# Kernel tuning notes

Hardware: AMD Instinct MI355X
Metric: run time of the kernel (lower is better)

Reference implementation:

```python
import jax, jax.numpy as jnp
import numpy as np

# ---- fixed hyperparameters (match init_kwargs / internal constants) ----
N_INP, N_HID = 96, 2048
DT = 0.075
GAMMA, EPSILON = 2.7, 4.7
RHO = 0.99
INPUT_SCALING = 1.0
LIF_TAU_M = 0.5
SPIKE_GAIN = 5.0
THETA_LIF, THETA_RF = 1.0, 1.0
ALPHA, BETA = 0.0, 0.0   # fixed internally (reset scaling disabled)
TAU_REF = 0.25


def setup_inputs() -> dict:
    key = jax.random.key(0)
    k_x, k_x2h, k_h2h, k_b = jax.random.split(key, 4)
    x = jax.random.normal(k_x, (32, 1024, N_INP), dtype=jnp.float32)
    # x2h = rand(n_inp, n_hid) * input_scaling
    x2h = jax.random.uniform(k_x2h, (N_INP, N_HID), dtype=jnp.float32) * INPUT_SCALING
    # h2h = 2*(2*rand - 1), then spectral-norm scaled so spectral radius = rho
    h2h = 2.0 * (2.0 * jax.random.uniform(k_h2h, (N_HID, N_HID), dtype=jnp.float32) - 1.0)
    sr = float(np.max(np.abs(np.linalg.eigvals(np.asarray(h2h, dtype=np.float64)))))
    h2h = h2h * (RHO / sr)
    # bias = (rand*2 - 1)*0.2 + 0.05
    bias = (jax.random.uniform(k_b, (N_HID,), dtype=jnp.float32) * 2.0 - 1.0) * 0.2 + 0.05
    return {"x": x, "x2h": x2h, "h2h": h2h, "bias": bias}


def reference(x, x2h, h2h, bias):
    B, T, _ = x.shape
    dt = jnp.float32(DT)
    ref_decay = jnp.exp(jnp.float32(-DT / TAU_REF))
    zeros = jnp.zeros((B, N_HID), dtype=x.dtype)
    # carry: (hy, hz, s, lif_v, ref_period, spike_counts)
    init = (zeros, zeros, zeros, zeros, zeros, zeros)

    def step(carry, xt):
        hy, hz, s, lif_v, ref_period, cnt = carry
        input_current = xt @ x2h + s @ h2h + bias          # [B, n_hid]
        lif_v = lif_v + dt * (-lif_v / LIF_TAU_M + input_current)
        lif_s = (lif_v > THETA_LIF).astype(x.dtype)
        lif_v = lif_v - lif_s * THETA_LIF
        drive = SPIKE_GAIN * lif_s
        hz = hz + dt * (drive - GAMMA * hy - EPSILON * hz)
        hy = hy + dt * hz
        s = (hy - THETA_RF - ref_period > 0).astype(x.dtype)
        hy = hy * (1.0 - s * ALPHA)
        hz = hz * (1.0 - s * BETA)
        ref_period = ref_period * ref_decay + s
        cnt = cnt + s
        return (hy, hz, s, lif_v, ref_period, cnt), None

    xt_seq = jnp.swapaxes(x, 0, 1)                          # [T, B, n_inp]
    (_, _, _, _, _, spike_counts), _ = jax.lax.scan(step, init, xt_seq)
    return spike_counts / jnp.float32(T)
```

## Files before the change

### kernel.cpp

```cpp
#include <hip/hip_runtime.h>
#include <cmath>

#define NH 2048
#define NI 96

__global__ __launch_bounds__(256) void xin_gemm(
    const float* __restrict__ A,
    const float* __restrict__ Bm,
    float* __restrict__ C)
{
    __shared__ float At[96][68];
    __shared__ float Bt[96][68];
    const int tid = threadIdx.x;
    const int rowBase = blockIdx.y * 64;
    const int colBase = blockIdx.x * 64;

    {
        const int r = tid >> 2;
        const int sub = tid & 3;
        const float4* Arow = reinterpret_cast<const float4*>(A + (size_t)(rowBase + r) * NI);
        #pragma unroll
        for (int q = 0; q < 6; ++q) {
            const int k4 = sub + 4 * q;
            float4 v = Arow[k4];
            At[k4 * 4 + 0][r] = v.x;
            At[k4 * 4 + 1][r] = v.y;
            At[k4 * 4 + 2][r] = v.z;
            At[k4 * 4 + 3][r] = v.w;
        }
    }
    {
        const int c4 = tid & 15;
        const int k0 = tid >> 4;
        #pragma unroll
        for (int g = 0; g < 6; ++g) {
            const int kk = k0 + 16 * g;
            float4 v = *reinterpret_cast<const float4*>(Bm + (size_t)kk * NH + colBase + c4 * 4);
            *reinterpret_cast<float4*>(&Bt[kk][c4 * 4]) = v;
        }
    }
    __syncthreads();

    const int ty = tid >> 4, tx = tid & 15;
    float acc[4][4] = {};
    #pragma unroll 8
    for (int kk = 0; kk < 96; ++kk) {
        float4 a = *reinterpret_cast<const float4*>(&At[kk][ty * 4]);
        float4 b = *reinterpret_cast<const float4*>(&Bt[kk][tx * 4]);
        acc[0][0] += a.x * b.x; acc[0][1] += a.x * b.y; acc[0][2] += a.x * b.z; acc[0][3] += a.x * b.w;
        acc[1][0] += a.y * b.x; acc[1][1] += a.y * b.y; acc[1][2] += a.y * b.z; acc[1][3] += a.y * b.w;
        acc[2][0] += a.z * b.x; acc[2][1] += a.z * b.y; acc[2][2] += a.z * b.z; acc[2][3] += a.z * b.w;
        acc[3][0] += a.w * b.x; acc[3][1] += a.w * b.y; acc[3][2] += a.w * b.z; acc[3][3] += a.w * b.w;
    }
    #pragma unroll
    for (int i = 0; i < 4; ++i) {
        float4 o;
        o.x = acc[i][0]; o.y = acc[i][1]; o.z = acc[i][2]; o.w = acc[i][3];
        *reinterpret_cast<float4*>(C + (size_t)(rowBase + ty * 4 + i) * NH + colBase + tx * 4) = o;
    }
}

template <int USE_XIN>
__global__ __launch_bounds__(512) void esn_seq(
    const float* __restrict__ xin,
    const float* __restrict__ x,
    const float* __restrict__ x2h,
    const float* __restrict__ h2h,
    const float* __restrict__ bias,
    float* __restrict__ out,
    int T)
{
    const int b = blockIdx.x;
    const int tid = threadIdx.x;
    const int n0 = tid * 4;
    const int wv = tid >> 6;
    const int lane = tid & 63;

    __shared__ alignas(16) int list[NH];
    __shared__ alignas(16) int wcnt[8];
    __shared__ float xt[NI];
    __shared__ alignas(16) float xstage[2][4][NH];

    constexpr float DT = 0.075f;
    constexpr float TAU_M = 0.5f;
    constexpr float GGAMMA = 2.7f;
    constexpr float GEPS = 4.7f;
    constexpr float GAIN = 5.0f;
    const float ref_decay = expf(-0.075f / 0.25f);

    float lv[4] = {0.f, 0.f, 0.f, 0.f};
    float hy[4] = {0.f, 0.f, 0.f, 0.f};
    float hz[4] = {0.f, 0.f, 0.f, 0.f};
    float rf[4] = {0.f, 0.f, 0.f, 0.f};
    float cnt[4] = {0.f, 0.f, 0.f, 0.f};
    float bs[4];
    {
        const float4 b4 = *reinterpret_cast<const float4*>(&bias[n0]);
        bs[0] = b4.x; bs[1] = b4.y; bs[2] = b4.z; bs[3] = b4.w;
    }
    int nact = 0;

    const float* __restrict__ xrow = USE_XIN ? (xin + (size_t)b * T * NH + n0) : xin;

    float4 P0, P1, P2, P3;

    if (USE_XIN) {
        #pragma unroll
        for (int r = 0; r < 4; ++r) {
            float4 v = *reinterpret_cast<const float4*>(xrow + (size_t)r * NH);
            *reinterpret_cast<float4*>(&xstage[0][r][n0]) = v;
        }
        P0 = *reinterpret_cast<const float4*>(xrow + (size_t)4 * NH);
        P1 = *reinterpret_cast<const float4*>(xrow + (size_t)5 * NH);
        P2 = *reinterpret_cast<const float4*>(xrow + (size_t)6 * NH);
        P3 = *reinterpret_cast<const float4*>(xrow + (size_t)7 * NH);
    } else {
        if (tid < NI) xt[tid] = x[(size_t)b * T * NI + tid];
    }
    __syncthreads();

    const unsigned long long below = (1ull << lane) - 1ull;
    const unsigned long long lo32 = 0xFFFFFFFFull;
    const unsigned long long mb = (lane >= 32) ? (below & ~lo32) : below;

    const int4* __restrict__ L4 = reinterpret_cast<const int4*>(list);

#define ISSUE(St, grp) do {                                                              \
        I##St = L4[(grp)];                                                               \
        const float* pr0 = h2h + (size_t)__builtin_amdgcn_readfirstlane(I##St.x) * NH;   \
        const float* pr1 = h2h + (size_t)__builtin_amdgcn_readfirstlane(I##St.y) * NH;   \
        const float* pr2 = h2h + (size_t)__builtin_amdgcn_readfirstlane(I##St.z) * NH;   \
        const float* pr3 = h2h + (size_t)__builtin_amdgcn_readfirstlane(I##St.w) * NH;   \
        W##St##_0 = *reinterpret_cast<const float4*>(pr0 + n0);                          \
        W##St##_1 = *reinterpret_cast<const float4*>(pr1 + n0);                          \
        W##St##_2 = *reinterpret_cast<const float4*>(pr2 + n0);                          \
        W##St##_3 = *reinterpret_cast<const float4*>(pr3 + n0);                          \
    } while (0)
#define ACC(St) do {                                                                  \
        a0[0] += W##St##_0.x; a0[1] += W##St##_0.y; a0[2] += W##St##_0.z; a0[3] += W##St##_0.w; \
        a1[0] += W##St##_1.x; a1[1] += W##St##_1.y; a1[2] += W##St##_1.z; a1[3] += W##St##_1.w; \
        a2[0] += W##St##_2.x; a2[1] += W##St##_2.y; a2[2] += W##St##_2.z; a2[3] += W##St##_2.w; \
        a3[0] += W##St##_3.x; a3[1] += W##St##_3.y; a3[2] += W##St##_3.z; a3[3] += W##St##_3.w; \
    } while (0)

    for (int t = 0; t < T; ++t) {
        float4 xi;
        if (USE_XIN) xi = *reinterpret_cast<const float4*>(&xstage[(t >> 2) & 1][t & 3][n0]);

        float a0[4] = {0.f, 0.f, 0.f, 0.f};
        float a1[4] = {0.f, 0.f, 0.f, 0.f};
        float a2[4] = {0.f, 0.f, 0.f, 0.f};
        float a3[4] = {0.f, 0.f, 0.f, 0.f};

        const int n4 = nact & ~3;
        const int G = n4 >> 2;
        const int tc = nact - n4;

        int4 I0, I1, I2, I3;
        float4 W0_0, W0_1, W0_2, W0_3;
        float4 W1_0, W1_1, W1_2, W1_3;
        float4 W2_0, W2_1, W2_2, W2_3;
        float4 W3_0, W3_1, W3_2, W3_3;

        if (0 < G) ISSUE(0, 0);
        if (1 < G) ISSUE(1, 1);
        if (2 < G) ISSUE(2, 2);
        if (3 < G) ISSUE(3, 3);
        float4 tw0, tw1, tw2;
        if (tc > 0) {
            const float* p = h2h + (size_t)__builtin_amdgcn_readfirstlane(list[n4]) * NH;
            tw0 = *reinterpret_cast<const float4*>(p + n0);
        }
        if (tc > 1) {
            const float* p = h2h + (size_t)__builtin_amdgcn_readfirstlane(list[n4 + 1]) * NH;
            tw1 = *reinterpret_cast<const float4*>(p + n0);
        }
        if (tc > 2) {
            const float* p = h2h + (size_t)__builtin_amdgcn_readfirstlane(list[n4 + 2]) * NH;
            tw2 = *reinterpret_cast<const float4*>(p + n0);
        }

        int g = 0;
        for (; g + 4 <= G; g += 4) {
            const bool r0 = (g + 4 < G), r1 = (g + 5 < G), r2 = (g + 6 < G), r3 = (g + 7 < G);
            ACC(0); if (r0) ISSUE(0, g + 4);
            ACC(1); if (r1) ISSUE(1, g + 5);
            ACC(2); if (r2) ISSUE(2, g + 6);
            ACC(3); if (r3) ISSUE(3, g + 7);
        }
        if (g + 0 < G) ACC(0);
        if (g + 1 < G) ACC(1);
        if (g + 2 < G) ACC(2);
        if (tc > 0) { a0[0] += tw0.x; a0[1] += tw0.y; a0[2] += tw0.z; a0[3] += tw0.w; }
        if (tc > 1) { a0[0] += tw1.x; a0[1] += tw1.y; a0[2] += tw1.z; a0[3] += tw1.w; }
        if (tc > 2) { a0[0] += tw2.x; a0[1] += tw2.y; a0[2] += tw2.z; a0[3] += tw2.w; }

        float ic[4];
        if (USE_XIN) {
            const float xiv[4] = {xi.x, xi.y, xi.z, xi.w};
            #pragma unroll
            for (int c = 0; c < 4; ++c) {
                const float rec = (a0[c] + a1[c]) + (a2[c] + a3[c]);
                ic[c] = (xiv[c] + rec) + bs[c];
            }
        } else {
            float m[4] = {0.f, 0.f, 0.f, 0.f};
            for (int i = 0; i < NI; ++i) {
                const float xv = xt[i];
                const float4 w = *reinterpret_cast<const float4*>(&x2h[(size_t)i * NH + n0]);
                m[0] += xv * w.x; m[1] += xv * w.y; m[2] += xv * w.z; m[3] += xv * w.w;
            }
            #pragma unroll
            for (int c = 0; c < 4; ++c) {
                const float rec = (a0[c] + a1[c]) + (a2[c] + a3[c]);
                ic[c] = (m[c] + rec) + bs[c];
            }
        }

        float s[4];
        #pragma unroll
        for (int c = 0; c < 4; ++c) {
            lv[c] = lv[c] + DT * (-lv[c] / TAU_M + ic[c]);
            const float ls = lv[c] > 1.0f ? 1.0f : 0.0f;
            lv[c] -= ls;
            hz[c] = hz[c] + DT * ((GAIN * ls - GGAMMA * hy[c]) - GEPS * hz[c]);
            hy[c] = hy[c] + DT * hz[c];
            s[c] = ((hy[c] - 1.0f) - rf[c]) > 0.0f ? 1.0f : 0.0f;
            rf[c] = rf[c] * ref_decay + s[c];
            cnt[c] += s[c];
        }

        const unsigned long long ba = __ballot(s[0] > 0.0f);
        const unsigned long long bb = __ballot(s[1] > 0.0f);
        const unsigned long long bc = __ballot(s[2] > 0.0f);
        const unsigned long long bd = __ballot(s[3] > 0.0f);
        if (lane == 0)
            wcnt[wv] = (int)(__popcll(ba) + __popcll(bb) + __popcll(bc) + __popcll(bd));

        if (USE_XIN && ((t & 3) == 3)) {
            const int bufW = ((t >> 2) + 1) & 1;
            *reinterpret_cast<float4*>(&xstage[bufW][0][n0]) = P0;
            *reinterpret_cast<float4*>(&xstage[bufW][1][n0]) = P1;
            *reinterpret_cast<float4*>(&xstage[bufW][2][n0]) = P2;
            *reinterpret_cast<float4*>(&xstage[bufW][3][n0]) = P3;
            const int cNext = (t >> 2) + 2;
            if (cNext * 4 + 3 < T) {
                P0 = *reinterpret_cast<const float4*>(xrow + (size_t)(cNext * 4 + 0) * NH);
                P1 = *reinterpret_cast<const float4*>(xrow + (size_t)(cNext * 4 + 1) * NH);
                P2 = *reinterpret_cast<const float4*>(xrow + (size_t)(cNext * 4 + 2) * NH);
                P3 = *reinterpret_cast<const float4*>(xrow + (size_t)(cNext * 4 + 3) * NH);
            }
        }
        __syncthreads();

        const int4 c0 = *reinterpret_cast<const int4*>(&wcnt[0]);
        const int4 c1 = *reinterpret_cast<const int4*>(&wcnt[4]);
        int pre = 0;
        pre += (wv > 0) ? c0.x : 0;
        pre += (wv > 1) ? c0.y : 0;
        pre += (wv > 2) ? c0.z : 0;
        pre += (wv > 3) ? c0.w : 0;
        pre += (wv > 4) ? c1.x : 0;
        pre += (wv > 5) ? c1.y : 0;
        pre += (wv > 6) ? c1.z : 0;
        const int tot = ((c0.x + c0.y) + (c0.z + c0.w)) + ((c1.x + c1.y) + (c1.z + c1.w));

        const int gaLo = (int)__popcll(ba & lo32);
        const int gbLo = (int)__popcll(bb & lo32);
        const int gcLo = (int)__popcll(bc & lo32);
        const int gdLo = (int)__popcll(bd & lo32);
        const int g0 = gaLo + gcLo;
        const int g1 = gbLo + gdLo;
        const int g2 = (int)(__popcll(ba) + __popcll(bc)) - g0;
        const int base02 = (lane < 32) ? 0 : (g0 + g1);
        const int base13 = (lane < 32) ? g0 : ((g0 + g1) + g2);
        const int pa = (int)__popcll(ba & mb);
        const int pb = (int)__popcll(bb & mb);
        const int pc = (int)__popcll(bc & mb);
        const int pd = (int)__popcll(bd & mb);
        const int o02 = pre + base02 + pa + pc;
        const int o13 = pre + base13 + pb + pd;
        if (s[0] > 0.0f) list[o02] = n0;
        if (s[2] > 0.0f) list[o02 + (int)((ba >> lane) & 1ull)] = n0 + 2;
        if (s[1] > 0.0f) list[o13] = n0 + 1;
        if (s[3] > 0.0f) list[o13 + (int)((bb >> lane) & 1ull)] = n0 + 3;
        nact = tot;
        if (!USE_XIN) {
            if (t + 1 < T && tid < NI) xt[tid] = x[((size_t)b * T + (t + 1)) * NI + tid];
        }
        __syncthreads();
    }
#undef ISSUE
#undef ACC

    float4 o;
    o.x = cnt[0] / (float)T;
    o.y = cnt[1] / (float)T;
    o.z = cnt[2] / (float)T;
    o.w = cnt[3] / (float)T;
    *reinterpret_cast<float4*>(out + (size_t)b * NH + n0) = o;
}

extern "C" void kernel_launch(void* const* d_in, const int* in_sizes, int n_in,
                              void* d_out, int out_size, void* d_ws, size_t ws_size,
                              hipStream_t stream) {
    const float* x    = (const float*)d_in[0];
    const float* x2h  = (const float*)d_in[1];
    const float* h2h  = (const float*)d_in[2];
    const float* bias = (const float*)d_in[3];
    float* out = (float*)d_out;

    const int M = in_sizes[0] / NI;
    const int T = 1024;
    const int B = M / T;

    const size_t xin_bytes = (size_t)M * NH * sizeof(float);
    if (ws_size >= xin_bytes) {
        float* xin = (float*)d_ws;
        dim3 grid(NH / 64, M / 64);
        xin_gemm<<<grid, 256, 0, stream>>>(x, x2h, xin);
        esn_seq<1><<<B, 512, 0, stream>>>(xin, x, x2h, h2h, bias, out, T);
    } else {
        esn_seq<0><<<B, 512, 0, stream>>>(x , x, x2h, h2h, bias, out, T);
    }
}
```

Baseline: 1.122 ms.

## Process two batch sequences per workgroup with interleaved sparse gathers

```diff
diff --git a/kernel.cpp b/kernel.cpp
--- a/kernel.cpp
+++ b/kernel.cpp
@@ -61,7 +61,340 @@
 }
 
 template <int USE_XIN>
-__global__ __launch_bounds__(512) void esn_seq(
+__global__ __launch_bounds__(512, 2) void esn_dual(
+    const float* __restrict__ xin,
+    const float* __restrict__ x,
+    const float* __restrict__ x2h,
+    const float* __restrict__ h2h,
+    const float* __restrict__ bias,
+    float* __restrict__ out,
+    int T)
+{
+    const int tid = threadIdx.x;
+    const int n0 = tid * 4;
+    const int wv = tid >> 6;
+    const int lane = tid & 63;
+    const int b0 = blockIdx.x * 2;
+
+    __shared__ alignas(16) int list[2][NH];
+    __shared__ alignas(16) int wcnt[2][8];
+    __shared__ float xt[2][NI];
+    __shared__ alignas(16) float xstage[2][2][2][NH];
+
+    constexpr float DT = 0.075f;
+    constexpr float TAU_M = 0.5f;
+    constexpr float GGAMMA = 2.7f;
+    constexpr float GEPS = 4.7f;
+    constexpr float GAIN = 5.0f;
+    const float ref_decay = expf(-0.075f / 0.25f);
+
+    float lvA[4] = {0,0,0,0}, hyA[4] = {0,0,0,0}, hzA[4] = {0,0,0,0};
+    float rfA[4] = {0,0,0,0}, cntA[4] = {0,0,0,0};
+    float lvB[4] = {0,0,0,0}, hyB[4] = {0,0,0,0}, hzB[4] = {0,0,0,0};
+    float rfB[4] = {0,0,0,0}, cntB[4] = {0,0,0,0};
+    float bs[4];
+    {
+        const float4 b4 = *reinterpret_cast<const float4*>(&bias[n0]);
+        bs[0] = b4.x; bs[1] = b4.y; bs[2] = b4.z; bs[3] = b4.w;
+    }
+    int nactA = 0, nactB = 0;
+
+    const float* __restrict__ xrowA = USE_XIN ? (xin + (size_t)b0 * T * NH + n0) : xin;
+    const float* __restrict__ xrowB = USE_XIN ? (xin + (size_t)(b0 + 1) * T * NH + n0) : xin;
+
+    float4 PA0, PA1, PB0, PB1;
+
+    if (USE_XIN) {
+        *reinterpret_cast<float4*>(&xstage[0][0][0][n0]) = *reinterpret_cast<const float4*>(xrowA + 0 * NH);
+        *reinterpret_cast<float4*>(&xstage[0][0][1][n0]) = *reinterpret_cast<const float4*>(xrowA + 1 * NH);
+        *reinterpret_cast<float4*>(&xstage[1][0][0][n0]) = *reinterpret_cast<const float4*>(xrowB + 0 * NH);
+        *reinterpret_cast<float4*>(&xstage[1][0][1][n0]) = *reinterpret_cast<const float4*>(xrowB + 1 * NH);
+        PA0 = *reinterpret_cast<const float4*>(xrowA + 2 * NH);
+        PA1 = *reinterpret_cast<const float4*>(xrowA + 3 * NH);
+        PB0 = *reinterpret_cast<const float4*>(xrowB + 2 * NH);
+        PB1 = *reinterpret_cast<const float4*>(xrowB + 3 * NH);
+    } else {
+        if (tid < NI) {
+            xt[0][tid] = x[(size_t)b0 * T * NI + tid];
+            xt[1][tid] = x[(size_t)(b0 + 1) * T * NI + tid];
+        }
+    }
+    __syncthreads();
+
+    const unsigned long long below = (1ull << lane) - 1ull;
+    const unsigned long long lo32 = 0xFFFFFFFFull;
+    const unsigned long long mb = (lane >= 32) ? (below & ~lo32) : below;
+
+    const int4* __restrict__ L4A = reinterpret_cast<const int4*>(&list[0][0]);
+    const int4* __restrict__ L4B = reinterpret_cast<const int4*>(&list[1][0]);
+
+#define ISSUE2(St, i) do {                                                               \
+        const int bt_ = ((i) < m2) ? ((i) & 1) : extraBt;                                \
+        const int gr_ = ((i) < m2) ? ((i) >> 1) : (mG + (i) - m2);                       \
+        BT##St = bt_;                                                                    \
+        I##St = bt_ ? L4B[gr_] : L4A[gr_];                                               \
+        const float* pr0 = h2h + (size_t)__builtin_amdgcn_readfirstlane(I##St.x) * NH;   \
+        const float* pr1 = h2h + (size_t)__builtin_amdgcn_readfirstlane(I##St.y) * NH;   \
+        const float* pr2 = h2h + (size_t)__builtin_amdgcn_readfirstlane(I##St.z) * NH;   \
+        const float* pr3 = h2h + (size_t)__builtin_amdgcn_readfirstlane(I##St.w) * NH;   \
+        W##St##_0 = *reinterpret_cast<const float4*>(pr0 + n0);                          \
+        W##St##_1 = *reinterpret_cast<const float4*>(pr1 + n0);                          \
+        W##St##_2 = *reinterpret_cast<const float4*>(pr2 + n0);                          \
+        W##St##_3 = *reinterpret_cast<const float4*>(pr3 + n0);                          \
+    } while (0)
+#define ACC2(St) do {                                                                    \
+        if (BT##St == 0) {                                                               \
+            aA0[0] += W##St##_0.x; aA0[1] += W##St##_0.y; aA0[2] += W##St##_0.z; aA0[3] += W##St##_0.w; \
+            aA1[0] += W##St##_1.x; aA1[1] += W##St##_1.y; aA1[2] += W##St##_1.z; aA1[3] += W##St##_1.w; \
+            aA2[0] += W##St##_2.x; aA2[1] += W##St##_2.y; aA2[2] += W##St##_2.z; aA2[3] += W##St##_2.w; \
+            aA3[0] += W##St##_3.x; aA3[1] += W##St##_3.y; aA3[2] += W##St##_3.z; aA3[3] += W##St##_3.w; \
+        } else {                                                                         \
+            aB0[0] += W##St##_0.x; aB0[1] += W##St##_0.y; aB0[2] += W##St##_0.z; aB0[3] += W##St##_0.w; \
+            aB1[0] += W##St##_1.x; aB1[1] += W##St##_1.y; aB1[2] += W##St##_1.z; aB1[3] += W##St##_1.w; \
+            aB2[0] += W##St##_2.x; aB2[1] += W##St##_2.y; aB2[2] += W##St##_2.z; aB2[3] += W##St##_2.w; \
+            aB3[0] += W##St##_3.x; aB3[1] += W##St##_3.y; aB3[2] += W##St##_3.z; aB3[3] += W##St##_3.w; \
+        }                                                                                \
+    } while (0)
+
+    for (int t = 0; t < T; ++t) {
+        float4 xiA, xiB;
+        if (USE_XIN) {
+            xiA = *reinterpret_cast<const float4*>(&xstage[0][(t >> 1) & 1][t & 1][n0]);
+            xiB = *reinterpret_cast<const float4*>(&xstage[1][(t >> 1) & 1][t & 1][n0]);
+        }
+
+        float aA0[4] = {0,0,0,0}, aA1[4] = {0,0,0,0}, aA2[4] = {0,0,0,0}, aA3[4] = {0,0,0,0};
+        float aB0[4] = {0,0,0,0}, aB1[4] = {0,0,0,0}, aB2[4] = {0,0,0,0}, aB3[4] = {0,0,0,0};
+
+        const int n4A = nactA & ~3, GA = n4A >> 2, tcA = nactA - n4A;
+        const int n4B = nactB & ~3, GB = n4B >> 2, tcB = nactB - n4B;
+        const int mG = (GA < GB) ? GA : GB;
+        const int m2 = 2 * mG;
+        const int NT = GA + GB;
+        const int extraBt = (GA > GB) ? 0 : 1;
+
+        int4 I0, I1, I2, I3;
+        int BT0, BT1, BT2, BT3;
+        float4 W0_0, W0_1, W0_2, W0_3;
+        float4 W1_0, W1_1, W1_2, W1_3;
+        float4 W2_0, W2_1, W2_2, W2_3;
+        float4 W3_0, W3_1, W3_2, W3_3;
+
+        if (0 < NT) ISSUE2(0, 0);
+        if (1 < NT) ISSUE2(1, 1);
+        if (2 < NT) ISSUE2(2, 2);
+        if (3 < NT) ISSUE2(3, 3);
+        float4 twA0, twA1, twA2, twB0, twB1, twB2;
+        if (tcA > 0) {
+            const float* p = h2h + (size_t)__builtin_amdgcn_readfirstlane(list[0][n4A]) * NH;
+            twA0 = *reinterpret_cast<const float4*>(p + n0);
+        }
+        if (tcA > 1) {
+            const float* p = h2h + (size_t)__builtin_amdgcn_readfirstlane(list[0][n4A + 1]) * NH;
+            twA1 = *reinterpret_cast<const float4*>(p + n0);
+        }
+        if (tcA > 2) {
+            const float* p = h2h + (size_t)__builtin_amdgcn_readfirstlane(list[0][n4A + 2]) * NH;
+            twA2 = *reinterpret_cast<const float4*>(p + n0);
+        }
+        if (tcB > 0) {
+            const float* p = h2h + (size_t)__builtin_amdgcn_readfirstlane(list[1][n4B]) * NH;
+            twB0 = *reinterpret_cast<const float4*>(p + n0);
+        }
+        if (tcB > 1) {
+            const float* p = h2h + (size_t)__builtin_amdgcn_readfirstlane(list[1][n4B + 1]) * NH;
+            twB1 = *reinterpret_cast<const float4*>(p + n0);
+        }
+        if (tcB > 2) {
+            const float* p = h2h + (size_t)__builtin_amdgcn_readfirstlane(list[1][n4B + 2]) * NH;
+            twB2 = *reinterpret_cast<const float4*>(p + n0);
+        }
+
+        int tk = 0;
+        for (; tk + 4 <= NT; tk += 4) {
+            ACC2(0); if (tk + 4 < NT) ISSUE2(0, tk + 4);
+            ACC2(1); if (tk + 5 < NT) ISSUE2(1, tk + 5);
+            ACC2(2); if (tk + 6 < NT) ISSUE2(2, tk + 6);
+            ACC2(3); if (tk + 7 < NT) ISSUE2(3, tk + 7);
+        }
+        if (tk + 0 < NT) ACC2(0);
+        if (tk + 1 < NT) ACC2(1);
+        if (tk + 2 < NT) ACC2(2);
+        if (tcA > 0) { aA0[0] += twA0.x; aA0[1] += twA0.y; aA0[2] += twA0.z; aA0[3] += twA0.w; }
+        if (tcA > 1) { aA0[0] += twA1.x; aA0[1] += twA1.y; aA0[2] += twA1.z; aA0[3] += twA1.w; }
+        if (tcA > 2) { aA0[0] += twA2.x; aA0[1] += twA2.y; aA0[2] += twA2.z; aA0[3] += twA2.w; }
+        if (tcB > 0) { aB0[0] += twB0.x; aB0[1] += twB0.y; aB0[2] += twB0.z; aB0[3] += twB0.w; }
+        if (tcB > 1) { aB0[0] += twB1.x; aB0[1] += twB1.y; aB0[2] += twB1.z; aB0[3] += twB1.w; }
+        if (tcB > 2) { aB0[0] += twB2.x; aB0[1] += twB2.y; aB0[2] += twB2.z; aB0[3] += twB2.w; }
+
+        float icA[4], icB[4];
+        if (USE_XIN) {
+            const float xivA[4] = {xiA.x, xiA.y, xiA.z, xiA.w};
+            const float xivB[4] = {xiB.x, xiB.y, xiB.z, xiB.w};
+            #pragma unroll
+            for (int c = 0; c < 4; ++c) {
+                const float recA = (aA0[c] + aA1[c]) + (aA2[c] + aA3[c]);
+                icA[c] = (xivA[c] + recA) + bs[c];
+                const float recB = (aB0[c] + aB1[c]) + (aB2[c] + aB3[c]);
+                icB[c] = (xivB[c] + recB) + bs[c];
+            }
+        } else {
+            float mA[4] = {0,0,0,0}, mB[4] = {0,0,0,0};
+            for (int i = 0; i < NI; ++i) {
+                const float xvA = xt[0][i];
+                const float xvB = xt[1][i];
+                const float4 w = *reinterpret_cast<const float4*>(&x2h[(size_t)i * NH + n0]);
+                mA[0] += xvA * w.x; mA[1] += xvA * w.y; mA[2] += xvA * w.z; mA[3] += xvA * w.w;
+                mB[0] += xvB * w.x; mB[1] += xvB * w.y; mB[2] += xvB * w.z; mB[3] += xvB * w.w;
+            }
+            #pragma unroll
+            for (int c = 0; c < 4; ++c) {
+                const float recA = (aA0[c] + aA1[c]) + (aA2[c] + aA3[c]);
+                icA[c] = (mA[c] + recA) + bs[c];
+                const float recB = (aB0[c] + aB1[c]) + (aB2[c] + aB3[c]);
+                icB[c] = (mB[c] + recB) + bs[c];
+            }
+        }
+
+        float sA[4], sB[4];
+        #pragma unroll
+        for (int c = 0; c < 4; ++c) {
+            lvA[c] = lvA[c] + DT * (-lvA[c] / TAU_M + icA[c]);
+            const float lsA = lvA[c] > 1.0f ? 1.0f : 0.0f;
+            lvA[c] -= lsA;
+            hzA[c] = hzA[c] + DT * ((GAIN * lsA - GGAMMA * hyA[c]) - GEPS * hzA[c]);
+            hyA[c] = hyA[c] + DT * hzA[c];
+            sA[c] = ((hyA[c] - 1.0f) - rfA[c]) > 0.0f ? 1.0f : 0.0f;
+            rfA[c] = rfA[c] * ref_decay + sA[c];
+            cntA[c] += sA[c];
+
+            lvB[c] = lvB[c] + DT * (-lvB[c] / TAU_M + icB[c]);
+            const float lsB = lvB[c] > 1.0f ? 1.0f : 0.0f;
+            lvB[c] -= lsB;
+            hzB[c] = hzB[c] + DT * ((GAIN * lsB - GGAMMA * hyB[c]) - GEPS * hzB[c]);
+            hyB[c] = hyB[c] + DT * hzB[c];
+            sB[c] = ((hyB[c] - 1.0f) - rfB[c]) > 0.0f ? 1.0f : 0.0f;
+            rfB[c] = rfB[c] * ref_decay + sB[c];
+            cntB[c] += sB[c];
+        }
+
+        const unsigned long long baA = __ballot(sA[0] > 0.0f);
+        const unsigned long long bbA = __ballot(sA[1] > 0.0f);
+        const unsigned long long bcA = __ballot(sA[2] > 0.0f);
+        const unsigned long long bdA = __ballot(sA[3] > 0.0f);
+        const unsigned long long baB = __ballot(sB[0] > 0.0f);
+        const unsigned long long bbB = __ballot(sB[1] > 0.0f);
+        const unsigned long long bcB = __ballot(sB[2] > 0.0f);
+        const unsigned long long bdB = __ballot(sB[3] > 0.0f);
+        if (lane == 0) {
+            wcnt[0][wv] = (int)(__popcll(baA) + __popcll(bbA) + __popcll(bcA) + __popcll(bdA));
+            wcnt[1][wv] = (int)(__popcll(baB) + __popcll(bbB) + __popcll(bcB) + __popcll(bdB));
+        }
+
+        if (USE_XIN && ((t & 1) == 1)) {
+            const int bufW = ((t >> 1) + 1) & 1;
+            *reinterpret_cast<float4*>(&xstage[0][bufW][0][n0]) = PA0;
+            *reinterpret_cast<float4*>(&xstage[0][bufW][1][n0]) = PA1;
+            *reinterpret_cast<float4*>(&xstage[1][bufW][0][n0]) = PB0;
+            *reinterpret_cast<float4*>(&xstage[1][bufW][1][n0]) = PB1;
+            const int cN = (t >> 1) + 2;
+            if (cN * 2 + 1 < T) {
+                PA0 = *reinterpret_cast<const float4*>(xrowA + (size_t)(cN * 2 + 0) * NH);
+                PA1 = *reinterpret_cast<const float4*>(xrowA + (size_t)(cN * 2 + 1) * NH);
+                PB0 = *reinterpret_cast<const float4*>(xrowB + (size_t)(cN * 2 + 0) * NH);
+                PB1 = *reinterpret_cast<const float4*>(xrowB + (size_t)(cN * 2 + 1) * NH);
+            }
+        }
+        __syncthreads();
+
+        {
+            const int4 c0 = *reinterpret_cast<const int4*>(&wcnt[0][0]);
+            const int4 c1 = *reinterpret_cast<const int4*>(&wcnt[0][4]);
+            int pre = 0;
+            pre += (wv > 0) ? c0.x : 0;
+            pre += (wv > 1) ? c0.y : 0;
+            pre += (wv > 2) ? c0.z : 0;
+            pre += (wv > 3) ? c0.w : 0;
+            pre += (wv > 4) ? c1.x : 0;
+            pre += (wv > 5) ? c1.y : 0;
+            pre += (wv > 6) ? c1.z : 0;
+            nactA = ((c0.x + c0.y) + (c0.z + c0.w)) + ((c1.x + c1.y) + (c1.z + c1.w));
+
+            const int gaLo = (int)__popcll(baA & lo32);
+            const int gbLo = (int)__popcll(bbA & lo32);
+            const int gcLo = (int)__popcll(bcA & lo32);
+            const int gdLo = (int)__popcll(bdA & lo32);
+            const int g0 = gaLo + gcLo;
+            const int g1 = gbLo + gdLo;
+            const int g2 = (int)(__popcll(baA) + __popcll(bcA)) - g0;
+            const int base02 = (lane < 32) ? 0 : (g0 + g1);
+            const int base13 = (lane < 32) ? g0 : ((g0 + g1) + g2);
+            const int pa = (int)__popcll(baA & mb);
+            const int pb = (int)__popcll(bbA & mb);
+            const int pc = (int)__popcll(bcA & mb);
+            const int pd = (int)__popcll(bdA & mb);
+            const int o02 = pre + base02 + pa + pc;
+            const int o13 = pre + base13 + pb + pd;
+            if (sA[0] > 0.0f) list[0][o02] = n0;
+            if (sA[2] > 0.0f) list[0][o02 + (int)((baA >> lane) & 1ull)] = n0 + 2;
+            if (sA[1] > 0.0f) list[0][o13] = n0 + 1;
+            if (sA[3] > 0.0f) list[0][o13 + (int)((bbA >> lane) & 1ull)] = n0 + 3;
+        }
+        {
+            const int4 c0 = *reinterpret_cast<const int4*>(&wcnt[1][0]);
+            const int4 c1 = *reinterpret_cast<const int4*>(&wcnt[1][4]);
+            int pre = 0;
+            pre += (wv > 0) ? c0.x : 0;
+            pre += (wv > 1) ? c0.y : 0;
+            pre += (wv > 2) ? c0.z : 0;
+            pre += (wv > 3) ? c0.w : 0;
+            pre += (wv > 4) ? c1.x : 0;
+            pre += (wv > 5) ? c1.y : 0;
+            pre += (wv > 6) ? c1.z : 0;
+            nactB = ((c0.x + c0.y) + (c0.z + c0.w)) + ((c1.x + c1.y) + (c1.z + c1.w));
+
+            const int gaLo = (int)__popcll(baB & lo32);
+            const int gbLo = (int)__popcll(bbB & lo32);
+            const int gcLo = (int)__popcll(bcB & lo32);
+            const int gdLo = (int)__popcll(bdB & lo32);
+            const int g0 = gaLo + gcLo;
+            const int g1 = gbLo + gdLo;
+            const int g2 = (int)(__popcll(baB) + __popcll(bcB)) - g0;
+            const int base02 = (lane < 32) ? 0 : (g0 + g1);
+            const int base13 = (lane < 32) ? g0 : ((g0 + g1) + g2);
+            const int pa = (int)__popcll(baB & mb);
+            const int pb = (int)__popcll(bbB & mb);
+            const int pc = (int)__popcll(bcB & mb);
+            const int pd = (int)__popcll(bdB & mb);
+            const int o02 = pre + base02 + pa + pc;
+            const int o13 = pre + base13 + pb + pd;
+            if (sB[0] > 0.0f) list[1][o02] = n0;
+            if (sB[2] > 0.0f) list[1][o02 + (int)((baB >> lane) & 1ull)] = n0 + 2;
+            if (sB[1] > 0.0f) list[1][o13] = n0 + 1;
+            if (sB[3] > 0.0f) list[1][o13 + (int)((bbB >> lane) & 1ull)] = n0 + 3;
+        }
+        if (!USE_XIN) {
+            if (t + 1 < T && tid < NI) {
+                xt[0][tid] = x[((size_t)b0 * T + (t + 1)) * NI + tid];
+                xt[1][tid] = x[((size_t)(b0 + 1) * T + (t + 1)) * NI + tid];
+            }
+        }
+        __syncthreads();
+    }
+#undef ISSUE2
+#undef ACC2
+
+    float4 oA, oB;
+    oA.x = cntA[0] / (float)T; oA.y = cntA[1] / (float)T;
+    oA.z = cntA[2] / (float)T; oA.w = cntA[3] / (float)T;
+    oB.x = cntB[0] / (float)T; oB.y = cntB[1] / (float)T;
+    oB.z = cntB[2] / (float)T; oB.w = cntB[3] / (float)T;
+    *reinterpret_cast<float4*>(out + (size_t)b0 * NH + n0) = oA;
+    *reinterpret_cast<float4*>(out + (size_t)(b0 + 1) * NH + n0) = oB;
+}
+
+template <int USE_XIN>
+__global__ __launch_bounds__(512) void esn_seq1(
     const float* __restrict__ xin,
     const float* __restrict__ x,
     const float* __restrict__ x2h,
@@ -88,11 +421,8 @@
     constexpr float GAIN = 5.0f;
     const float ref_decay = expf(-0.075f / 0.25f);
 
-    float lv[4] = {0.f, 0.f, 0.f, 0.f};
-    float hy[4] = {0.f, 0.f, 0.f, 0.f};
-    float hz[4] = {0.f, 0.f, 0.f, 0.f};
-    float rf[4] = {0.f, 0.f, 0.f, 0.f};
-    float cnt[4] = {0.f, 0.f, 0.f, 0.f};
+    float lv[4] = {0,0,0,0}, hy[4] = {0,0,0,0}, hz[4] = {0,0,0,0};
+    float rf[4] = {0,0,0,0}, cnt[4] = {0,0,0,0};
     float bs[4];
     {
         const float4 b4 = *reinterpret_cast<const float4*>(&bias[n0]);
@@ -101,7 +431,6 @@
     int nact = 0;
 
     const float* __restrict__ xrow = USE_XIN ? (xin + (size_t)b * T * NH + n0) : xin;
-
     float4 P0, P1, P2, P3;
 
     if (USE_XIN) {
@@ -122,10 +451,9 @@
     const unsigned long long below = (1ull << lane) - 1ull;
     const unsigned long long lo32 = 0xFFFFFFFFull;
     const unsigned long long mb = (lane >= 32) ? (below & ~lo32) : below;
-
     const int4* __restrict__ L4 = reinterpret_cast<const int4*>(list);
 
-#define ISSUE(St, grp) do {                                                              \
+#define ISSUE1(St, grp) do {                                                             \
         I##St = L4[(grp)];                                                               \
         const float* pr0 = h2h + (size_t)__builtin_amdgcn_readfirstlane(I##St.x) * NH;   \
         const float* pr1 = h2h + (size_t)__builtin_amdgcn_readfirstlane(I##St.y) * NH;   \
@@ -136,7 +464,7 @@
         W##St##_2 = *reinterpret_cast<const float4*>(pr2 + n0);                          \
         W##St##_3 = *reinterpret_cast<const float4*>(pr3 + n0);                          \
     } while (0)
-#define ACC(St) do {                                                                  \
+#define ACC1(St) do {                                                                    \
         a0[0] += W##St##_0.x; a0[1] += W##St##_0.y; a0[2] += W##St##_0.z; a0[3] += W##St##_0.w; \
         a1[0] += W##St##_1.x; a1[1] += W##St##_1.y; a1[2] += W##St##_1.z; a1[3] += W##St##_1.w; \
         a2[0] += W##St##_2.x; a2[1] += W##St##_2.y; a2[2] += W##St##_2.z; a2[3] += W##St##_2.w; \
@@ -147,11 +475,7 @@
         float4 xi;
         if (USE_XIN) xi = *reinterpret_cast<const float4*>(&xstage[(t >> 2) & 1][t & 3][n0]);
 
-        float a0[4] = {0.f, 0.f, 0.f, 0.f};
-        float a1[4] = {0.f, 0.f, 0.f, 0.f};
-        float a2[4] = {0.f, 0.f, 0.f, 0.f};
-        float a3[4] = {0.f, 0.f, 0.f, 0.f};
-
+        float a0[4] = {0,0,0,0}, a1[4] = {0,0,0,0}, a2[4] = {0,0,0,0}, a3[4] = {0,0,0,0};
         const int n4 = nact & ~3;
         const int G = n4 >> 2;
         const int tc = nact - n4;
@@ -162,10 +486,10 @@
         float4 W2_0, W2_1, W2_2, W2_3;
         float4 W3_0, W3_1, W3_2, W3_3;
 
-        if (0 < G) ISSUE(0, 0);
-        if (1 < G) ISSUE(1, 1);
-        if (2 < G) ISSUE(2, 2);
-        if (3 < G) ISSUE(3, 3);
+        if (0 < G) ISSUE1(0, 0);
+        if (1 < G) ISSUE1(1, 1);
+        if (2 < G) ISSUE1(2, 2);
+        if (3 < G) ISSUE1(3, 3);
         float4 tw0, tw1, tw2;
         if (tc > 0) {
             const float* p = h2h + (size_t)__builtin_amdgcn_readfirstlane(list[n4]) * NH;
@@ -183,14 +507,14 @@
         int g = 0;
         for (; g + 4 <= G; g += 4) {
             const bool r0 = (g + 4 < G), r1 = (g + 5 < G), r2 = (g + 6 < G), r3 = (g + 7 < G);
-            ACC(0); if (r0) ISSUE(0, g + 4);
-            ACC(1); if (r1) ISSUE(1, g + 5);
-            ACC(2); if (r2) ISSUE(2, g + 6);
-            ACC(3); if (r3) ISSUE(3, g + 7);
-        }
-        if (g + 0 < G) ACC(0);
-        if (g + 1 < G) ACC(1);
-        if (g + 2 < G) ACC(2);
+            ACC1(0); if (r0) ISSUE1(0, g + 4);
+            ACC1(1); if (r1) ISSUE1(1, g + 5);
+            ACC1(2); if (r2) ISSUE1(2, g + 6);
+            ACC1(3); if (r3) ISSUE1(3, g + 7);
+        }
+        if (g + 0 < G) ACC1(0);
+        if (g + 1 < G) ACC1(1);
+        if (g + 2 < G) ACC1(2);
         if (tc > 0) { a0[0] += tw0.x; a0[1] += tw0.y; a0[2] += tw0.z; a0[3] += tw0.w; }
         if (tc > 1) { a0[0] += tw1.x; a0[1] += tw1.y; a0[2] += tw1.z; a0[3] += tw1.w; }
         if (tc > 2) { a0[0] += tw2.x; a0[1] += tw2.y; a0[2] += tw2.z; a0[3] += tw2.w; }
@@ -204,7 +528,7 @@
                 ic[c] = (xiv[c] + rec) + bs[c];
             }
         } else {
-            float m[4] = {0.f, 0.f, 0.f, 0.f};
+            float m[4] = {0,0,0,0};
             for (int i = 0; i < NI; ++i) {
                 const float xv = xt[i];
                 const float4 w = *reinterpret_cast<const float4*>(&x2h[(size_t)i * NH + n0]);
@@ -290,8 +614,8 @@
         }
         __syncthreads();
     }
-#undef ISSUE
-#undef ACC
+#undef ISSUE1
+#undef ACC1
 
     float4 o;
     o.x = cnt[0] / (float)T;
@@ -319,8 +643,16 @@
         float* xin = (float*)d_ws;
         dim3 grid(NH / 64, M / 64);
         xin_gemm<<<grid, 256, 0, stream>>>(x, x2h, xin);
-        esn_seq<1><<<B, 512, 0, stream>>>(xin, x, x2h, h2h, bias, out, T);
+        if ((B & 1) == 0 && B >= 2) {
+            esn_dual<1><<<B / 2, 512, 0, stream>>>(xin, x, x2h, h2h, bias, out, T);
+        } else {
+            esn_seq1<1><<<B, 512, 0, stream>>>(xin, x, x2h, h2h, bias, out, T);
+        }
     } else {
-        esn_seq<0><<<B, 512, 0, stream>>>(x , x, x2h, h2h, bias, out, T);
+        if ((B & 1) == 0 && B >= 2) {
+            esn_dual<0><<<B / 2, 512, 0, stream>>>(x , x, x2h, h2h, bias, out, T);
+        } else {
+            esn_seq1<0><<<B, 512, 0, stream>>>(x , x, x2h, h2h, bias, out, T);
+        }
     }
 }
```

Measured after the change: 1.801 ms. 1.6x slower.
